# Optimization experiments

Measured on AMD Instinct MI355X. Metric: run time of the kernel, lower is better.

The kernel has to match this reference:

```python
import jax, jax.numpy as jnp
import numpy as np

EPS = 1e-5


def setup_inputs() -> dict:
    key = jax.random.key(0)
    ks = jax.random.split(key, 5)
    b, c, L = 2, 512, 1024
    x = jax.random.normal(ks[0], (b, c, L), dtype=jnp.float32)
    gamma = jnp.ones((c,), dtype=jnp.float32)
    beta = jnp.zeros((c,), dtype=jnp.float32)
    w_qkv = jax.random.normal(ks[1], (3 * c, c), dtype=jnp.float32) * (1.0 / np.sqrt(c))
    b_qkv = jax.random.normal(ks[2], (3 * c,), dtype=jnp.float32) * 0.02
    # NOTE: original zero-inits proj_out; we use random weights for a
    # non-degenerate correctness baseline (same math, different init values).
    w_proj = jax.random.normal(ks[3], (c, c), dtype=jnp.float32) * (1.0 / np.sqrt(c))
    b_proj = jnp.zeros((c,), dtype=jnp.float32)
    return {"x": x, "gamma": gamma, "beta": beta, "w_qkv": w_qkv,
            "b_qkv": b_qkv, "w_proj": w_proj, "b_proj": b_proj, "num_heads": 8}


def reference(x, gamma, beta, w_qkv, b_qkv, w_proj, b_proj, num_heads):
    b, c, L = x.shape
    nh = int(num_heads)
    hd = c // nh
    # BatchNorm1d, training mode: stats over (batch, length) per channel
    mean = jnp.mean(x, axis=(0, 2), keepdims=True)
    var = jnp.mean((x - mean) ** 2, axis=(0, 2), keepdims=True)  # biased var
    xn = (x - mean) * jax.lax.rsqrt(var + EPS)
    xn = xn * gamma[None, :, None] + beta[None, :, None]
    # 1x1 conv == matmul over channel axis: (b, 3c, L)
    qkv = jnp.einsum('oc,bcl->bol', w_qkv, xn) + b_qkv[None, :, None]
    # Faithful (quirky) layout: (b, 3*nh, hd, L) -> (b, hd, L, 3*nh)
    qkv = qkv.reshape(b, 3 * nh, hd, L).transpose(0, 2, 3, 1)
    q, k, v = jnp.split(qkv, 3, axis=-1)  # each (b, hd, L, nh)
    scale = (3 * nh) ** (-0.5)  # original scales by qkv's last dim before chunk
    # scores: (b, hd, T, T) -- 'heads' axis is hd due to the layout quirk
    w = jax.nn.softmax(jnp.einsum('bhtd,bhfd->bhtf', q * scale, k), axis=-1)
    a = jnp.einsum('bhtf,bhfd->bhtd', w, v)  # (b, hd, L, nh)
    h = a.transpose(0, 3, 1, 2).reshape(b, c, L)
    h = jnp.einsum('oc,bcl->bol', w_proj, h) + b_proj[None, :, None]
    return x + h
```

## Files before the change

### kernel.cpp

```cpp
#include <hip/hip_runtime.h>
#include <hip/hip_bf16.h>
#include <cstddef>
#include <cstdint>

#define B_ 2
#define C_ 512
#define L_ 1024
#define NH_ 8
#define HD_ 64
#define OC_ 1536

typedef short short8 __attribute__((ext_vector_type(8)));
typedef short short4v __attribute__((ext_vector_type(4)));
typedef float f32x4 __attribute__((ext_vector_type(4)));
typedef __fp16 f16x4 __attribute__((ext_vector_type(4)));
typedef __fp16 f16x2 __attribute__((ext_vector_type(2)));

__device__ inline float bf_bits_to_f32(unsigned short u) {
  union { unsigned u32; float f; } c; c.u32 = ((unsigned)u) << 16; return c.f;
}
__device__ inline short f32_to_bf_bits(float f) {
  union { float f; unsigned u; } c; c.f = f;
  return (short)((c.u + 0x7FFFu + ((c.u >> 16) & 1u)) >> 16);
}

__device__ __forceinline__ float fexp2_fast(float y) {
  union { unsigned u; float f; } v;
  v.u = (unsigned)fmaf(y, 8388608.0f, 1065055000.0f);
  return v.f;
}

__device__ __forceinline__ void gl2lds16(const short* g, short* l) {
  __builtin_amdgcn_global_load_lds(
      (const __attribute__((address_space(1))) unsigned*)(const void*)g,
      (__attribute__((address_space(3))) unsigned*)(void*)l, 16, 0, 0);
}

__global__ __launch_bounds__(256) void prep_kernel(
    const float* __restrict__ x, const float* __restrict__ gamma,
    const float* __restrict__ beta, const float* __restrict__ w_qkv,
    const float* __restrict__ w_proj,
    float* __restrict__ s_out, float* __restrict__ t_out,
    short* __restrict__ wq16, short* __restrict__ wpp16)
{
  const int bid = blockIdx.x;
  const int tid = threadIdx.x;
  if (bid < 512) {
    const int ch = bid;
    const float4 v0 = *(const float4*)(x + (size_t)ch * L_ + tid * 4);
    const float4 v1 = *(const float4*)(x + (size_t)(C_ + ch) * L_ + tid * 4);
    float s1 = v0.x + v0.y + v0.z + v0.w + v1.x + v1.y + v1.z + v1.w;
    float s2 = v0.x*v0.x + v0.y*v0.y + v0.z*v0.z + v0.w*v0.w
             + v1.x*v1.x + v1.y*v1.y + v1.z*v1.z + v1.w*v1.w;
    #pragma unroll
    for (int off = 32; off > 0; off >>= 1) {
      s1 += __shfl_down(s1, off);
      s2 += __shfl_down(s2, off);
    }
    __shared__ float r1[4], r2[4];
    const int wid = tid >> 6, lane = tid & 63;
    if (lane == 0) { r1[wid] = s1; r2[wid] = s2; }
    __syncthreads();
    if (tid == 0) {
      const float S1 = r1[0] + r1[1] + r1[2] + r1[3];
      const float S2 = r2[0] + r2[1] + r2[2] + r2[3];
      const float invN = 1.f / (float)(B_ * L_);
      const float mean = S1 * invN;
      const float var  = S2 * invN - mean * mean;
      const float rstd = rsqrtf(var + 1e-5f);
      const float sc = gamma[ch] * rstd;
      s_out[ch] = sc;
      t_out[ch] = beta[ch] - mean * sc;
    }
  } else if (bid < 704) {
    const int base = (bid - 512) * 4096 + tid * 16;
    #pragma unroll
    for (int it = 0; it < 2; ++it) {
      const float4 a0 = *(const float4*)(w_qkv + base + it * 8);
      const float4 a1 = *(const float4*)(w_qkv + base + it * 8 + 4);
      short8 v;
      v[0] = f32_to_bf_bits(a0.x); v[1] = f32_to_bf_bits(a0.y);
      v[2] = f32_to_bf_bits(a0.z); v[3] = f32_to_bf_bits(a0.w);
      v[4] = f32_to_bf_bits(a1.x); v[5] = f32_to_bf_bits(a1.y);
      v[6] = f32_to_bf_bits(a1.z); v[7] = f32_to_bf_bits(a1.w);
      *(short8*)(wq16 + base + it * 8) = v;
    }
  } else {
    #pragma unroll
    for (int grp = 0; grp < 4; ++grp) {
      const int idx = (bid - 704) * 4096 + tid * 16 + grp * 4;
      const int o = idx >> 9, cp = idx & 511;
      short4v v;
      #pragma unroll
      for (int j = 0; j < 4; ++j) {
        const int c = ((cp + j) & 7) * 64 + ((cp + j) >> 3);
        v[j] = f32_to_bf_bits(w_proj[(size_t)o * C_ + c]);
      }
      *(short4v*)(wpp16 + (size_t)o * C_ + cp) = v;
    }
  }
}

__global__ __launch_bounds__(256) void xt_kernel(
    const float* __restrict__ x, const float* __restrict__ s,
    const float* __restrict__ t, short* __restrict__ xT)
{
  __shared__ float T[64][65];
  const int t0 = blockIdx.x * 64, c0 = blockIdx.y * 64, b = blockIdx.z;
  const int tid = threadIdx.x;
  const float* xp = x + (size_t)b * C_ * L_;
  #pragma unroll
  for (int it = 0; it < 4; ++it) {
    const int idx = it * 256 + tid;
    const int rr = idx >> 4, c4 = (idx & 15) * 4;
    const float4 v = *(const float4*)(xp + (size_t)(c0 + rr) * L_ + t0 + c4);
    const float sc = s[c0 + rr], tc = t[c0 + rr];
    T[rr][c4 + 0] = fmaf(v.x, sc, tc);
    T[rr][c4 + 1] = fmaf(v.y, sc, tc);
    T[rr][c4 + 2] = fmaf(v.z, sc, tc);
    T[rr][c4 + 3] = fmaf(v.w, sc, tc);
  }
  __syncthreads();
  #pragma unroll
  for (int it = 0; it < 4; ++it) {
    const int idx = it * 256 + tid;
    const int tt_ = idx >> 4, cc4 = (idx & 15) * 4;
    short4v o;
    #pragma unroll
    for (int j = 0; j < 4; ++j) o[j] = f32_to_bf_bits(T[cc4 + j][tt_]);
    *(short4v*)(xT + ((size_t)b * L_ + t0 + tt_) * C_ + c0 + cc4) = o;
  }
}

template <int MR, int NR, bool OUT_BF16>
__global__ __launch_bounds__(256) void gemm_bt16_kernel(
    const short* __restrict__ A, const short* __restrict__ B,
    const float* __restrict__ bias, const float* __restrict__ res,
    void* __restrict__ Cv, int M, int N, int K,
    size_t sB, size_t sC, size_t sR)
{
  constexpr int BM = MR * 32, BN = NR * 32;
  __shared__ short As[BM * 64];
  __shared__ short Bs[BN * 64];
  const int tid = threadIdx.x;
  const int l = tid & 63, w = tid >> 6;
  const int wr = w >> 1, wc = w & 1;
  const int ll = l & 15;
  const int n0 = blockIdx.x * BN, m0 = blockIdx.y * BM, bz = blockIdx.z;
  const short* Bg = B + (size_t)bz * sB;
  f32x4 acc[MR][NR] = {};

  for (int k0 = 0; k0 < K; k0 += 64) {
    #pragma unroll
    for (int it = 0; it < BM / 32; ++it) {
      const int row0 = w * (BM / 4) + it * 8;
      const int row = row0 + (l >> 3), sl = l & 7;
      gl2lds16(A + (size_t)(m0 + row) * K + k0 + ((sl ^ (row & 7)) * 8),
               As + row0 * 64);
    }
    #pragma unroll
    for (int it = 0; it < BN / 32; ++it) {
      const int row0 = w * (BN / 4) + it * 8;
      const int row = row0 + (l >> 3), sl = l & 7;
      gl2lds16(Bg + (size_t)(n0 + row) * K + k0 + ((sl ^ (row & 7)) * 8),
               Bs + row0 * 64);
    }
    __syncthreads();
    #pragma unroll
    for (int kk = 0; kk < 2; ++kk) {
      short8 af[MR], bfg[NR];
      const int sd = kk * 4 + (l >> 4);
      #pragma unroll
      for (int m = 0; m < MR; ++m) {
        const int ra = wr * MR * 16 + m * 16 + ll;
        af[m] = *(const short8*)(As + ra * 64 + (sd ^ (ra & 7)) * 8);
      }
      #pragma unroll
      for (int n = 0; n < NR; ++n) {
        const int rb = wc * NR * 16 + n * 16 + ll;
        bfg[n] = *(const short8*)(Bs + rb * 64 + (sd ^ (rb & 7)) * 8);
      }
      #pragma unroll
      for (int m = 0; m < MR; ++m)
        #pragma unroll
        for (int n = 0; n < NR; ++n)
          acc[m][n] = __builtin_amdgcn_mfma_f32_16x16x32_bf16(
              af[m], bfg[n], acc[m][n], 0, 0, 0);
    }
    __syncthreads();
  }

  const int rg4 = (l >> 4) * 4;
  __hip_bfloat16* Cb = (__hip_bfloat16*)Cv + (size_t)bz * sC;
  float* Cf = (float*)Cv + (size_t)bz * sC;
  const float* Rp = res + (size_t)bz * sR;
  #pragma unroll
  for (int m = 0; m < MR; ++m) {
    #pragma unroll
    for (int reg = 0; reg < 4; ++reg) {
      const int gm = m0 + wr * MR * 16 + m * 16 + rg4 + reg;
      const float bv = bias[gm];
      #pragma unroll
      for (int n = 0; n < NR; ++n) {
        const int gn = n0 + wc * NR * 16 + n * 16 + ll;
        float v = acc[m][n][reg] + bv;
        if (OUT_BF16) {
          Cb[(size_t)gm * N + gn] = __hip_bfloat16_raw{(unsigned short)f32_to_bf_bits(v)};
        } else {
          v += Rp[(size_t)gm * N + gn];
          Cf[(size_t)gm * N + gn] = v;
        }
      }
    }
  }
}

__global__ __launch_bounds__(256, 4) void attn_kernel(
    const __hip_bfloat16* __restrict__ qkv, short* __restrict__ hT)
{
  __shared__ __fp16 Klds[1024 * 8];
  __shared__ __fp16 Vlds[9 * 1032];

  const int tq = blockIdx.x, d = blockIdx.y, b = blockIdx.z;
  const int tid = threadIdx.x;
  const int w = tid >> 6, l = tid & 63;
  const int hi = l >> 4, ll = l & 15;
  const int t0 = tq * 128 + w * 32;
  const short* base = (const short*)qkv + (size_t)b * OC_ * L_;
  short* KldsS = (short*)Klds;
  short* VldsS = (short*)Vlds;

  #pragma unroll
  for (int it = 0; it < 4; ++it) {
    const int f = it * 256 + tid;
    unsigned u[4];
    #pragma unroll
    for (int e = 0; e < 4; ++e) {
      const f16x2 p = __builtin_amdgcn_cvt_pkrtz(
          bf_bits_to_f32((unsigned short)base[(size_t)((8 + 2*e)   * HD_ + d) * L_ + f]),
          bf_bits_to_f32((unsigned short)base[(size_t)((8 + 2*e+1) * HD_ + d) * L_ + f]));
      u[e] = __builtin_bit_cast(unsigned, p);
    }
    uint4 uu; uu.x = u[0]; uu.y = u[1]; uu.z = u[2]; uu.w = u[3];
    *(uint4*)(KldsS + f * 8) = uu;
  }
  #pragma unroll
  for (int it = 0; it < 4; ++it) {
    const int i = it * 256 + tid;
    const int g = i >> 7, fs = i & 127;
    const short8 v = *(const short8*)(
        base + (size_t)((16 + g) * HD_ + d) * L_ + fs * 8);
    unsigned u[4];
    #pragma unroll
    for (int e = 0; e < 4; ++e) {
      const f16x2 p = __builtin_amdgcn_cvt_pkrtz(
          bf_bits_to_f32((unsigned short)v[2 * e]),
          bf_bits_to_f32((unsigned short)v[2 * e + 1]));
      u[e] = __builtin_bit_cast(unsigned, p);
    }
    uint4 uu; uu.x = u[0]; uu.y = u[1]; uu.z = u[2]; uu.w = u[3];
    *(uint4*)(VldsS + g * 1032 + fs * 8) = uu;
  }
  {
    uint2 ones; ones.x = 0x3C003C00u; ones.y = 0x3C003C00u;
    *(uint2*)(VldsS + 8 * 1032 + tid * 4) = ones;
  }

  f16x4 bQ[2] = {};
  if (l < 32) {
    const int g0 = 4 * hi;
    #pragma unroll
    for (int tt = 0; tt < 2; ++tt) {
      const int t = t0 + tt * 16 + ll;
      float q[4];
      #pragma unroll
      for (int j = 0; j < 4; ++j)
        q[j] = bf_bits_to_f32(
                   (unsigned short)base[(size_t)((g0 + j) * HD_ + d) * L_ + t]) *
               0.29448889f;
      const f16x2 a = __builtin_amdgcn_cvt_pkrtz(q[0], q[1]);
      const f16x2 bb = __builtin_amdgcn_cvt_pkrtz(q[2], q[3]);
      union { f16x4 v; uint2 u; } m;
      m.u.x = __builtin_bit_cast(unsigned, a);
      m.u.y = __builtin_bit_cast(unsigned, bb);
      bQ[tt] = m.v;
    }
  }

  __syncthreads();

  const int vrow = (ll < 9) ? ll : 8;
  const f32x4 z4 = {0.f, 0.f, 0.f, 0.f};
  f32x4 accA[2] = {}, accB[2] = {};
  const __fp16* akB = Klds + ll * 8 + 4 * (hi & 1);
  const __fp16* avB = Vlds + vrow * 1032 + 4 * hi;

  #pragma unroll
  for (int c = 0; c < 8; ++c) {
    #pragma unroll
    for (int ft = 0; ft < 8; ++ft) {
      const f16x4 ak = *(const f16x4*)(akB + c * 1024 + ft * 128);
      const f16x4 av = *(const f16x4*)(avB + c * 128 + ft * 16);
      #pragma unroll
      for (int tt = 0; tt < 2; ++tt) {
        const f32x4 s = __builtin_amdgcn_mfma_f32_16x16x16f16(
            ak, bQ[tt], z4, 0, 0, 0);
        const f16x2 p0 = __builtin_amdgcn_cvt_pkrtz(fexp2_fast(s[0]),
                                                    fexp2_fast(s[1]));
        const f16x2 p1 = __builtin_amdgcn_cvt_pkrtz(fexp2_fast(s[2]),
                                                    fexp2_fast(s[3]));
        union { f16x4 v; uint2 u; } bp;
        bp.u.x = __builtin_bit_cast(unsigned, p0);
        bp.u.y = __builtin_bit_cast(unsigned, p1);
        if (c & 1)
          accB[tt] = __builtin_amdgcn_mfma_f32_16x16x16f16(av, bp.v, accB[tt], 0, 0, 0);
        else
          accA[tt] = __builtin_amdgcn_mfma_f32_16x16x16f16(av, bp.v, accA[tt], 0, 0, 0);
      }
    }
  }

  f32x4 accO[2];
  #pragma unroll
  for (int tt = 0; tt < 2; ++tt) accO[tt] = accA[tt] + accB[tt];

  __syncthreads();
  short* Olds = KldsS;
  #pragma unroll
  for (int nt = 0; nt < 2; ++nt) {
    const float sum = __shfl(accO[nt][0], 32 + ll);
    const float inv = 1.f / sum;
    if (hi < 2) {
      const int tl = w * 32 + nt * 16 + ll;
      #pragma unroll
      for (int reg = 0; reg < 4; ++reg)
        Olds[tl * 8 + hi * 4 + reg] = f32_to_bf_bits(accO[nt][reg] * inv);
    }
  }
  __syncthreads();
  if (tid < 128) {
    const short8 ov = *(const short8*)(Olds + tid * 8);
    *(short8*)(hT + ((size_t)b * L_ + tq * 128 + tid) * C_ + d * 8) = ov;
  }
}

extern "C" void kernel_launch(void* const* d_in, const int* in_sizes, int n_in,
                              void* d_out, int out_size, void* d_ws, size_t ws_size,
                              hipStream_t stream) {
  (void)in_sizes; (void)n_in; (void)out_size; (void)ws_size;
  const float* x      = (const float*)d_in[0];
  const float* gamma  = (const float*)d_in[1];
  const float* beta   = (const float*)d_in[2];
  const float* w_qkv  = (const float*)d_in[3];
  const float* b_qkv  = (const float*)d_in[4];
  const float* w_proj = (const float*)d_in[5];
  const float* b_proj = (const float*)d_in[6];
  float* out = (float*)d_out;
  char* wsb = (char*)d_ws;

  float* s_buf = (float*)(wsb + 0);
  float* t_buf = (float*)(wsb + 2048);
  short* wq16  = (short*)(wsb + 4096);
  short* wpp16 = (short*)(wsb + 4096 + 1572864);
  short* xT    = (short*)(wsb + 4096 + 2097152);
  short* qkv   = (short*)(wsb + 4096 + 4194304);
  short* hT    = (short*)(wsb + 4096 + 10485760);

  hipLaunchKernelGGL(prep_kernel, dim3(768), dim3(256), 0, stream,
                     x, gamma, beta, w_qkv, w_proj, s_buf, t_buf, wq16, wpp16);
  hipLaunchKernelGGL(xt_kernel, dim3(L_ / 64, C_ / 64, B_), dim3(256), 0, stream,
                     x, s_buf, t_buf, xT);
  hipLaunchKernelGGL((gemm_bt16_kernel<2, 2, true>),
                     dim3(L_ / 64, OC_ / 64, B_), dim3(256), 0, stream,
                     wq16, xT, b_qkv, (const float*)nullptr, (void*)qkv,
                     OC_, L_, C_, (size_t)L_ * C_, (size_t)OC_ * L_, (size_t)0);
  hipLaunchKernelGGL(attn_kernel, dim3(8, HD_, B_), dim3(256), 0, stream,
                     (const __hip_bfloat16*)qkv, hT);
  hipLaunchKernelGGL((gemm_bt16_kernel<1, 2, false>),
                     dim3(L_ / 64, C_ / 32, B_), dim3(256), 0, stream,
                     wpp16, hT, b_proj, x, (void*)out,
                     C_, L_, C_, (size_t)L_ * C_, (size_t)C_ * L_, (size_t)C_ * L_);
}
```

Before: 47.77 us.

## Add relayout kernel producing fp16 K/Q/V buffers for attention loads

Adds a separate kernel that converts the bf16 qkv output into fp16 interleaved K and pre-scaled Q buffers plus contiguous V rows, once per (batch, d). The attention kernel then loads K straight into LDS with direct global-to-LDS copies and reads Q/V without conversion. This removes the redundant strided gather and conversion that each of the 8 query-tile blocks repeated. The cost is an extra launch and an extra round-trip of about 6MB through global memory.

```diff
diff --git a/kernel.cpp b/kernel.cpp
--- a/kernel.cpp
+++ b/kernel.cpp
@@ -215,8 +215,57 @@
   }
 }
 
+__global__ __launch_bounds__(256) void relayout_kernel(
+    const __hip_bfloat16* __restrict__ qkv,
+    short* __restrict__ Kb, short* __restrict__ Qb, short* __restrict__ Vb)
+{
+  const int fh = blockIdx.x, d = blockIdx.y, b = blockIdx.z;
+  const int tid = threadIdx.x;
+  const short* base = (const short*)qkv + (size_t)b * OC_ * L_;
+  const size_t bd = (size_t)b * 64 + d;
+
+  #pragma unroll
+  for (int i = 0; i < 2; ++i) {
+    const int f = fh * 512 + i * 256 + tid;
+    unsigned ku[4], qu[4];
+    #pragma unroll
+    for (int e = 0; e < 4; ++e) {
+      const f16x2 kp = __builtin_amdgcn_cvt_pkrtz(
+          bf_bits_to_f32((unsigned short)base[(size_t)((8 + 2*e)   * HD_ + d) * L_ + f]),
+          bf_bits_to_f32((unsigned short)base[(size_t)((8 + 2*e+1) * HD_ + d) * L_ + f]));
+      ku[e] = __builtin_bit_cast(unsigned, kp);
+      const f16x2 qp = __builtin_amdgcn_cvt_pkrtz(
+          bf_bits_to_f32((unsigned short)base[(size_t)((2*e)   * HD_ + d) * L_ + f]) * 0.29448889f,
+          bf_bits_to_f32((unsigned short)base[(size_t)((2*e+1) * HD_ + d) * L_ + f]) * 0.29448889f);
+      qu[e] = __builtin_bit_cast(unsigned, qp);
+    }
+    uint4 kk; kk.x = ku[0]; kk.y = ku[1]; kk.z = ku[2]; kk.w = ku[3];
+    uint4 qq; qq.x = qu[0]; qq.y = qu[1]; qq.z = qu[2]; qq.w = qu[3];
+    *(uint4*)(Kb + (bd * 1024 + f) * 8) = kk;
+    *(uint4*)(Qb + (bd * 1024 + f) * 8) = qq;
+  }
+  #pragma unroll
+  for (int it = 0; it < 2; ++it) {
+    const int i = it * 256 + tid;
+    const int g = fh * 4 + (i >> 7), fs = i & 127;
+    const short8 v = *(const short8*)(
+        base + (size_t)((16 + g) * HD_ + d) * L_ + fs * 8);
+    unsigned u[4];
+    #pragma unroll
+    for (int e = 0; e < 4; ++e) {
+      const f16x2 p = __builtin_amdgcn_cvt_pkrtz(
+          bf_bits_to_f32((unsigned short)v[2 * e]),
+          bf_bits_to_f32((unsigned short)v[2 * e + 1]));
+      u[e] = __builtin_bit_cast(unsigned, p);
+    }
+    uint4 uu; uu.x = u[0]; uu.y = u[1]; uu.z = u[2]; uu.w = u[3];
+    *(uint4*)(Vb + ((bd * 8 + g) * 1024 + fs * 8)) = uu;
+  }
+}
+
 __global__ __launch_bounds__(256, 4) void attn_kernel(
-    const __hip_bfloat16* __restrict__ qkv, short* __restrict__ hT)
+    const short* __restrict__ Kb, const short* __restrict__ Qb,
+    const short* __restrict__ Vb, short* __restrict__ hT)
 {
   __shared__ __fp16 Klds[1024 * 8];
   __shared__ __fp16 Vlds[9 * 1032];
@@ -226,65 +275,34 @@
   const int w = tid >> 6, l = tid & 63;
   const int hi = l >> 4, ll = l & 15;
   const int t0 = tq * 128 + w * 32;
-  const short* base = (const short*)qkv + (size_t)b * OC_ * L_;
+  const size_t bd = (size_t)b * 64 + d;
   short* KldsS = (short*)Klds;
   short* VldsS = (short*)Vlds;
 
-  #pragma unroll
-  for (int it = 0; it < 4; ++it) {
-    const int f = it * 256 + tid;
-    unsigned u[4];
-    #pragma unroll
-    for (int e = 0; e < 4; ++e) {
-      const f16x2 p = __builtin_amdgcn_cvt_pkrtz(
-          bf_bits_to_f32((unsigned short)base[(size_t)((8 + 2*e)   * HD_ + d) * L_ + f]),
-          bf_bits_to_f32((unsigned short)base[(size_t)((8 + 2*e+1) * HD_ + d) * L_ + f]));
-      u[e] = __builtin_bit_cast(unsigned, p);
-    }
-    uint4 uu; uu.x = u[0]; uu.y = u[1]; uu.z = u[2]; uu.w = u[3];
-    *(uint4*)(KldsS + f * 8) = uu;
+  {
+    const short* Ks = Kb + bd * 8192 + w * 2048;
+    short* Kd = KldsS + w * 2048;
+    #pragma unroll
+    for (int j = 0; j < 4; ++j)
+      gl2lds16(Ks + j * 512 + l * 8, Kd + j * 512);
   }
   #pragma unroll
   for (int it = 0; it < 4; ++it) {
     const int i = it * 256 + tid;
     const int g = i >> 7, fs = i & 127;
-    const short8 v = *(const short8*)(
-        base + (size_t)((16 + g) * HD_ + d) * L_ + fs * 8);
-    unsigned u[4];
-    #pragma unroll
-    for (int e = 0; e < 4; ++e) {
-      const f16x2 p = __builtin_amdgcn_cvt_pkrtz(
-          bf_bits_to_f32((unsigned short)v[2 * e]),
-          bf_bits_to_f32((unsigned short)v[2 * e + 1]));
-      u[e] = __builtin_bit_cast(unsigned, p);
-    }
-    uint4 uu; uu.x = u[0]; uu.y = u[1]; uu.z = u[2]; uu.w = u[3];
+    const uint4 uu = *(const uint4*)(Vb + ((bd * 8 + g) * 1024 + fs * 8));
     *(uint4*)(VldsS + g * 1032 + fs * 8) = uu;
   }
   {
     uint2 ones; ones.x = 0x3C003C00u; ones.y = 0x3C003C00u;
     *(uint2*)(VldsS + 8 * 1032 + tid * 4) = ones;
   }
-
   f16x4 bQ[2] = {};
   if (l < 32) {
-    const int g0 = 4 * hi;
-    #pragma unroll
-    for (int tt = 0; tt < 2; ++tt) {
-      const int t = t0 + tt * 16 + ll;
-      float q[4];
-      #pragma unroll
-      for (int j = 0; j < 4; ++j)
-        q[j] = bf_bits_to_f32(
-                   (unsigned short)base[(size_t)((g0 + j) * HD_ + d) * L_ + t]) *
-               0.29448889f;
-      const f16x2 a = __builtin_amdgcn_cvt_pkrtz(q[0], q[1]);
-      const f16x2 bb = __builtin_amdgcn_cvt_pkrtz(q[2], q[3]);
-      union { f16x4 v; uint2 u; } m;
-      m.u.x = __builtin_bit_cast(unsigned, a);
-      m.u.y = __builtin_bit_cast(unsigned, bb);
-      bQ[tt] = m.v;
-    }
+    #pragma unroll
+    for (int tt = 0; tt < 2; ++tt)
+      bQ[tt] = *(const f16x4*)((const __fp16*)Qb +
+                               (bd * 1024 + t0 + tt * 16 + ll) * 8 + 4 * hi);
   }
 
   __syncthreads();
@@ -365,6 +383,9 @@
   short* xT    = (short*)(wsb + 4096 + 2097152);
   short* qkv   = (short*)(wsb + 4096 + 4194304);
   short* hT    = (short*)(wsb + 4096 + 10485760);
+  short* Kb    = (short*)(wsb + 12587008);
+  short* Qb    = (short*)(wsb + 14684160);
+  short* Vb    = (short*)(wsb + 16781312);
 
   hipLaunchKernelGGL(prep_kernel, dim3(768), dim3(256), 0, stream,
                      x, gamma, beta, w_qkv, w_proj, s_buf, t_buf, wq16, wpp16);
@@ -374,8 +395,10 @@
                      dim3(L_ / 64, OC_ / 64, B_), dim3(256), 0, stream,
                      wq16, xT, b_qkv, (const float*)nullptr, (void*)qkv,
                      OC_, L_, C_, (size_t)L_ * C_, (size_t)OC_ * L_, (size_t)0);
+  hipLaunchKernelGGL(relayout_kernel, dim3(2, HD_, B_), dim3(256), 0, stream,
+                     (const __hip_bfloat16*)qkv, Kb, Qb, Vb);
   hipLaunchKernelGGL(attn_kernel, dim3(8, HD_, B_), dim3(256), 0, stream,
-                     (const __hip_bfloat16*)qkv, hT);
+                     Kb, Qb, Vb, hT);
   hipLaunchKernelGGL((gemm_bt16_kernel<1, 2, false>),
                      dim3(L_ / 64, C_ / 32, B_), dim3(256), 0, stream,
                      wpp16, hT, b_proj, x, (void*)out,
```

Result: slower. 50.71 us (+6.1%).
